# Optimization experiments

Hardware: AMD Instinct MI355X
Metric: run time of the kernel (lower is better)

Reference implementation:

```python
import jax, jax.numpy as jnp
import numpy as np

B, L, T, F, H, O = 4096, 50, 64, 3, 20, 16

def setup_inputs() -> dict:
    key = jax.random.key(0)
    ks = jax.random.split(key, 20)
    p = lambda k, s: jax.random.normal(k, s, jnp.float32) * 0.1
    inp = {
        'x': jax.random.normal(ks[0], (B, L, T, F), jnp.float32),
        'lengths': jax.random.randint(ks[1], (B, L), 0, T, jnp.int32),
        # LSTMCell params (torch gate order i,f,g,o)
        'w_ih': p(ks[2], (4 * H, F)), 'w_hh': p(ks[3], (4 * H, H)),
        'b_ih': p(ks[4], (4 * H,)), 'b_hh': p(ks[5], (4 * H,)),
        # layer-summary Linear(20,16)
        'w_lin': p(ks[6], (O, H)), 'b_lin': p(ks[7], (O,)),
        # ClassifyNet convs
        'c1_w': p(ks[8], (32, 16, 5)), 'c1_b': p(ks[9], (32,)),
        'c2_w': p(ks[10], (32, 32, 4)), 'c2_b': p(ks[11], (32,)),
        'c3_w': p(ks[12], (32, 32, 4)), 'c3_b': p(ks[13], (32,)),
        'fc1_w': p(ks[14], (16, 32 * 19)), 'fc1_b': p(ks[15], (16,)),
        'fc2_w': p(ks[16], (4, 16)), 'fc2_b': p(ks[17], (4,)),
    }
    return inp

def _conv1d(x, w, b, stride):
    y = jax.lax.conv_general_dilated(x, w, (stride,), 'VALID',
                                     dimension_numbers=('NCH', 'OIH', 'NCH'))
    return y + b[None, :, None]

def _lstm_last_h(xseq, lens, w_ih, w_hh, b_ih, b_hh):
    # xseq: [N,T,F] padded; lens: [N]. Masked batched LSTM, returns h at step len-1.
    N = xseq.shape[0]
    xT = jnp.swapaxes(xseq, 0, 1)  # [T,N,F]
    h0 = jnp.zeros((N, H), xseq.dtype)
    def step(carry, inp):
        h, c = carry
        x_t, t = inp
        gates = x_t @ w_ih.T + b_ih + h @ w_hh.T + b_hh
        i, f, g, o = jnp.split(gates, 4, axis=-1)
        c_new = jax.nn.sigmoid(f) * c + jax.nn.sigmoid(i) * jnp.tanh(g)
        h_new = jax.nn.sigmoid(o) * jnp.tanh(c_new)
        m = (t < lens)[:, None]
        return (jnp.where(m, h_new, h), jnp.where(m, c_new, c)), None
    (h, _), _ = jax.lax.scan(step, (h0, h0), (xT, jnp.arange(xT.shape[0])))
    return h

def reference(x, lengths, w_ih, w_hh, b_ih, b_hh, w_lin, b_lin,
              c1_w, c1_b, c2_w, c2_b, c3_w, c3_b, fc1_w, fc1_b, fc2_w, fc2_b):
    N = B * L
    xf = x.reshape(N, T, F)
    lens = lengths.reshape(N)
    h = _lstm_last_h(xf, lens, w_ih, w_hh, b_ih, b_hh)          # [N,20]
    summ = jax.nn.sigmoid(h @ w_lin.T + b_lin)                   # [N,16]
    summ = jnp.where((lens > 0)[:, None], summ, 0.0)             # empty layer -> zeros
    feat = jnp.swapaxes(summ.reshape(B, L, O), 1, 2)             # [B,16,50]
    y = jax.nn.relu(_conv1d(feat, c1_w, c1_b, 1))                # [B,32,46]
    y = jax.nn.relu(_conv1d(y, c2_w, c2_b, 2))                   # [B,32,22]
    y = jax.nn.relu(_conv1d(y, c3_w, c3_b, 1))                   # [B,32,19]
    y = y.reshape(B, 32 * 19)
    y = jax.nn.relu(y @ fc1_w.T + fc1_b)
    return y @ fc2_w.T + fc2_b                                   # [B,4]
```

## Files before the change

kernel.cpp:

```cpp
#include <hip/hip_runtime.h>
#include <cstdint>
#include <cstddef>

#define NB 4096
#define NL 50
#define NT 64
#define NF 3
#define NH 20
#define NO 16
#define NN (NB*NL)
#define SB 16
#define TS 16
#define HSTR 20
#define XSTR 8

typedef __attribute__((ext_vector_type(8))) short bf16x8;
typedef __attribute__((ext_vector_type(4))) float f32x4;

__device__ __forceinline__ float fsig(float z) {
    return __builtin_amdgcn_rcpf(1.0f + __expf(-z));
}
__device__ __forceinline__ unsigned short f2bf(float f) {
    unsigned int x = __float_as_uint(f);
    x = (x + 0x7fffu + ((x >> 16) & 1u)) >> 16;
    return (unsigned short)x;
}
__device__ __forceinline__ float bf2f(unsigned short u) {
    return __uint_as_float(((unsigned int)u) << 16);
}

__global__ __launch_bounds__(256) void hist_kernel(const int* __restrict__ lengths,
                                                   int* __restrict__ hist) {
    __shared__ int lh[64];
    int tid = threadIdx.x;
    if (tid < 64) lh[tid] = 0;
    __syncthreads();
    int n = blockIdx.x * 256 + tid;
    if (n < NN) {
        int len = lengths[n];
        len = len < 0 ? 0 : (len > 63 ? 63 : len);
        atomicAdd(&lh[len], 1);
    }
    __syncthreads();
    if (tid < 64 && lh[tid] != 0) atomicAdd(&hist[tid], lh[tid]);
}

__global__ void scan_kernel(const int* __restrict__ hist, int* __restrict__ cursor) {
    int l = threadIdx.x;
    int v = hist[l];
    int s = v;
#pragma unroll
    for (int d = 1; d < 64; d <<= 1) {
        int o = __shfl_up(s, d);
        if (l >= d) s += o;
    }
    cursor[l] = s - v;
}

__global__ __launch_bounds__(256) void scatter_kernel(const int* __restrict__ lengths,
                                                      int* __restrict__ cursor,
                                                      int* __restrict__ order,
                                                      int* __restrict__ len_s) {
    __shared__ int lcnt[64];
    __shared__ int lbase[64];
    int tid = threadIdx.x;
    if (tid < 64) lcnt[tid] = 0;
    __syncthreads();
    int n = blockIdx.x * 256 + tid;
    int len = 0, myrank = 0;
    if (n < NN) {
        len = lengths[n];
        len = len < 0 ? 0 : (len > 63 ? 63 : len);
        myrank = atomicAdd(&lcnt[len], 1);
    }
    __syncthreads();
    if (tid < 64 && lcnt[tid] != 0) lbase[tid] = atomicAdd(&cursor[tid], lcnt[tid]);
    __syncthreads();
    if (n < NN) {
        int pos = lbase[len] + myrank;
        order[pos] = n;
        len_s[pos] = len;
    }
}

__global__ void wfrag_kernel(const float* __restrict__ w_hh,
                             const float* __restrict__ b_ih,
                             const float* __restrict__ b_hh,
                             const float* __restrict__ w_ih,
                             unsigned int* __restrict__ wfrag) {
    int l = threadIdx.x;
    int m = l & 15, kg = l >> 4;
    for (int T = 0; T < 5; ++T) {
        int g = (m & 3) * 20 + T * 4 + (m >> 2);
        unsigned int hi[4], lo[4];
        for (int d = 0; d < 4; ++d) {
            unsigned int hw[2], lw[2];
            for (int e = 0; e < 2; ++e) {
                int k = kg * 8 + d * 2 + e;
                float v = 0.0f;
                if (k < 20)       v = w_hh[g * 20 + k];
                else if (k == 20) v = b_ih[g] + b_hh[g];
                else if (k <= 23) v = w_ih[g * 3 + (k - 21)];
                else if (k <= 26) v = w_ih[g * 3 + (k - 24)];
                unsigned short h16 = f2bf(v);
                float r = v - bf2f(h16);
                hw[e] = h16; lw[e] = f2bf(r);
            }
            hi[d] = hw[0] | (hw[1] << 16);
            lo[d] = lw[0] | (lw[1] << 16);
        }
        for (int d = 0; d < 4; ++d) {
            wfrag[(size_t)((T * 2 + 0) * 64 + l) * 4 + d] = hi[d];
            wfrag[(size_t)((T * 2 + 1) * 64 + l) * 4 + d] = lo[d];
        }
    }
}

#define LSTM_STEP(K, MASKED)                                                     \
    {                                                                            \
        uint2 ra_ = *(const uint2*)(p1 + (K) * st1);                             \
        uint2 rb_ = *(const uint2*)(p2 + (K) * st2);                             \
        union { uint4 u; bf16x8 v; } bb_;                                        \
        bb_.u = make_uint4(ra_.x, ra_.y, rb_.x, rb_.y);                          \
        f32x4 acc[5];                                                            \
        _Pragma("unroll")                                                        \
        for (int T = 0; T < 5; ++T) {                                            \
            f32x4 z4 = {0.f, 0.f, 0.f, 0.f};                                     \
            z4     = __builtin_amdgcn_mfma_f32_16x16x32_bf16(wf[2*T],   bb_.v, z4, 0, 0, 0); \
            acc[T] = __builtin_amdgcn_mfma_f32_16x16x32_bf16(wf[2*T+1], bb_.v, z4, 0, 0, 0); \
        }                                                                        \
        bool m_ = true;                                                          \
        if (MASKED) m_ = (t0 + (K)) < mylen;                                     \
        _Pragma("unroll")                                                        \
        for (int T = 0; T < 5; ++T) {                                            \
            float Ei = __expf(-acc[T][0]);                                       \
            float Ef = __expf(-acc[T][1]);                                       \
            float G  = __expf(acc[T][2] + acc[T][2]);                            \
            float Eo = __expf(-acc[T][3]);                                       \
            float Ai = 1.0f + Ei, Af = 1.0f + Ef, Bg = 1.0f + G;                 \
            float t1 = Ai * Bg;                                                  \
            float num = fmaf(G - 1.0f, Af, c5[T] * t1);                          \
            float cn  = num * __builtin_amdgcn_rcpf(t1 * Af);                    \
            float ce  = fminf(cn, 15.0f);                                        \
            float Ec  = __expf(ce + ce);                                         \
            float hn  = (Ec - 1.0f) *                                            \
                        __builtin_amdgcn_rcpf((1.0f + Eo) * (1.0f + Ec));        \
            if (m_) {                                                            \
                c5[T] = cn;                                                      \
                hbf[wid][hoff + T * 4] = f2bf(hn);                               \
            }                                                                    \
        }                                                                        \
    }

__global__ __launch_bounds__(256) void lstm_kernel(
    const float* __restrict__ x,
    const int*   __restrict__ len_s,
    const int*   __restrict__ order,
    const unsigned int* __restrict__ wfrag,
    const float* __restrict__ w_lin,
    const float* __restrict__ b_lin,
    float* __restrict__ feat)
{
    __shared__ __align__(16) unsigned short hbf[4][SB * HSTR];
    __shared__ __align__(16) unsigned short xbf[4][TS * SB * XSTR];
    __shared__ __align__(16) unsigned short zbuf[4][8];

    const int tid  = threadIdx.x;
    const int wid  = __builtin_amdgcn_readfirstlane(tid >> 6);
    const int lane = tid & 63;
    const int n16  = lane & 15;
    const int kg   = lane >> 4;
    const int base = ((gridDim.x - 1 - blockIdx.x) * 4 + wid) * SB;

    const int mylen   = len_s[base + n16];
    const int wavemin = len_s[base];
    const int wavemax = len_s[base + SB - 1];

    for (int i = lane; i < SB * HSTR; i += 64) hbf[wid][i] = 0;
    if (lane < 8) zbuf[wid][lane] = 0;
    for (int i = lane; i < TS * SB; i += 64) {
        xbf[wid][i * XSTR + 0] = 0x3F80;
        xbf[wid][i * XSTR + 7] = 0;
    }

    bf16x8 wf[10];
#pragma unroll
    for (int p = 0; p < 10; ++p) {
        union { uint4 i; bf16x8 v; } cv;
        cv.i = ((const uint4*)wfrag)[p * 64 + lane];
        wf[p] = cv.v;
    }

    int nown = order[base + n16];
    size_t gb[3]; int ssj[3], qqj[3];
#pragma unroll
    for (int j = 0; j < 3; ++j) {
        int e4 = lane + 64 * j;
        int ss = e4 / 12;
        int q  = e4 - 12 * ss;
        int ns = __shfl(nown, ss);
        gb[j] = (size_t)ns * (NT * NF) + q * 4;
        ssj[j] = ss; qqj[j] = q;
    }

    const unsigned short* hpw = &hbf[wid][n16 * HSTR];
    const unsigned short* p1 = (kg < 3) ? (hpw + kg * 8)
                                        : &xbf[wid][n16 * XSTR + 4];
    const unsigned short* p2 = (kg < 2) ? (hpw + kg * 8 + 4)
                             : (kg == 2 ? &xbf[wid][n16 * XSTR]
                                        : &zbuf[wid][0]);
    const int st1 = (kg == 3) ? SB * XSTR : 0;
    const int st2 = (kg == 2) ? SB * XSTR : 0;
    const int hoff = n16 * HSTR + kg;

    float c5[5];
#pragma unroll
    for (int j = 0; j < 5; ++j) c5[j] = 0.0f;

    if (wavemax > 0) {
        float4 vf[3];
#pragma unroll
        for (int j = 0; j < 3; ++j) vf[j] = *(const float4*)(x + gb[j]);

        for (int t0 = 0; t0 < wavemax; t0 += TS) {
#pragma unroll
            for (int j = 0; j < 3; ++j) {
                float fv4[4] = {vf[j].x, vf[j].y, vf[j].z, vf[j].w};
                int ss = ssj[j], q = qqj[j];
#pragma unroll
                for (int e = 0; e < 4; ++e) {
                    int fi = q * 4 + e;
                    int t  = fi / 3;
                    int cc = fi - 3 * t;
                    unsigned short hi = f2bf(fv4[e]);
                    unsigned short lo = f2bf(fv4[e] - bf2f(hi));
                    int bidx = (t * SB + ss) * XSTR;
                    xbf[wid][bidx + 1 + cc] = hi;
                    xbf[wid][bidx + 4 + cc] = lo;
                }
            }
            if (t0 + TS < wavemax) {
                size_t off = (size_t)(t0 + TS) * NF;
#pragma unroll
                for (int j = 0; j < 3; ++j)
                    vf[j] = *(const float4*)(x + gb[j] + off);
            }

            int kmax = wavemax - t0; if (kmax > TS) kmax = TS;
            int ku = wavemin - t0;
            ku = ku < 0 ? 0 : (ku > kmax ? kmax : ku);
            int k = 0;
            for (; k < ku; ++k)   LSTM_STEP(k, false)
            for (; k < kmax; ++k) LSTM_STEP(k, true)
        }
    }

    float hl[NH];
#pragma unroll
    for (int u = 0; u < NH; ++u) hl[u] = bf2f(hbf[wid][n16 * HSTR + u]);
    float4 res;
    if (mylen > 0) {
        float r4[4];
#pragma unroll
        for (int j = 0; j < 4; ++j) {
            int o = 4 * kg + j;
            float aa = b_lin[o];
#pragma unroll
            for (int kk = 0; kk < NH; ++kk) aa += w_lin[o * NH + kk] * hl[kk];
            r4[j] = fsig(aa);
        }
        res = make_float4(r4[0], r4[1], r4[2], r4[3]);
    } else {
        res = make_float4(0.f, 0.f, 0.f, 0.f);
    }
    *(float4*)(feat + (size_t)nown * NO + 4 * kg) = res;
}

__global__ __launch_bounds__(256) void head_kernel(
    const float* __restrict__ feat,
    const float* __restrict__ c1w, const float* __restrict__ c1b,
    const float* __restrict__ c2w, const float* __restrict__ c2b,
    const float* __restrict__ c3w, const float* __restrict__ c3b,
    const float* __restrict__ f1w, const float* __restrict__ f1b,
    const float* __restrict__ f2w, const float* __restrict__ f2b,
    float* __restrict__ out)
{
    const int b0  = blockIdx.x * 2;
    const int tid = threadIdx.x;
    const int p   = tid & 63;
    const int q   = __builtin_amdgcn_readfirstlane(tid >> 6);
    const int half = p >> 5;
    const int pp   = p & 31;

    __shared__ float sf[2][16 * 50];
    __shared__ float y1[2][32 * 46];
    __shared__ float y2[2][32 * 22];
    __shared__ float y3[2][32 * 19];
    __shared__ float r1[2][16];

    for (int i = tid; i < 2 * NL * NO; i += 256) {
        int bb = (i >= NL * NO) ? 1 : 0;
        int j = i - bb * (NL * NO);
        int l = j >> 4, o = j & 15;
        sf[bb][o * 50 + l] = feat[(size_t)(b0 + bb) * (NL * NO) + j];
    }
    __syncthreads();

    const int oc0 = q * 8;

#pragma unroll
    for (int bb = 0; bb < 2; ++bb) {
        if (p < 46) {
            float acc[8];
#pragma unroll
            for (int oc = 0; oc < 8; ++oc) acc[oc] = c1b[oc0 + oc];
#pragma unroll
            for (int ic = 0; ic < 16; ++ic) {
#pragma unroll
                for (int tap = 0; tap < 5; ++tap) {
                    float fv = sf[bb][ic * 50 + p + tap];
#pragma unroll
                    for (int oc = 0; oc < 8; ++oc)
                        acc[oc] += c1w[((oc0 + oc) * 16 + ic) * 5 + tap] * fv;
                }
            }
#pragma unroll
            for (int oc = 0; oc < 8; ++oc)
                y1[bb][(oc0 + oc) * 46 + p] = fmaxf(acc[oc], 0.0f);
        }
    }
    __syncthreads();

    if (pp < 22) {
        float acc[8];
#pragma unroll
        for (int oc = 0; oc < 8; ++oc) acc[oc] = c2b[oc0 + oc];
#pragma unroll
        for (int ic = 0; ic < 32; ++ic) {
#pragma unroll
            for (int tap = 0; tap < 4; ++tap) {
                float fv = y1[half][ic * 46 + 2 * pp + tap];
#pragma unroll
                for (int oc = 0; oc < 8; ++oc)
                    acc[oc] += c2w[((oc0 + oc) * 32 + ic) * 4 + tap] * fv;
            }
        }
#pragma unroll
        for (int oc = 0; oc < 8; ++oc)
            y2[half][(oc0 + oc) * 22 + pp] = fmaxf(acc[oc], 0.0f);
    }
    __syncthreads();

    if (pp < 19) {
        float acc[8];
#pragma unroll
        for (int oc = 0; oc < 8; ++oc) acc[oc] = c3b[oc0 + oc];
#pragma unroll
        for (int ic = 0; ic < 32; ++ic) {
#pragma unroll
            for (int tap = 0; tap < 4; ++tap) {
                float fv = y2[half][ic * 22 + pp + tap];
#pragma unroll
                for (int oc = 0; oc < 8; ++oc)
                    acc[oc] += c3w[((oc0 + oc) * 32 + ic) * 4 + tap] * fv;
            }
        }
#pragma unroll
        for (int oc = 0; oc < 8; ++oc)
            y3[half][(oc0 + oc) * 19 + pp] = fmaxf(acc[oc], 0.0f);
    }
    __syncthreads();

    if (q < 2) {
        int u  = p & 15;
        int qq = p >> 4;
        float acc = 0.0f;
        int k0 = qq * 152;
#pragma unroll 8
        for (int k = k0; k < k0 + 152; ++k) acc += f1w[u * 608 + k] * y3[q][k];
        acc += __shfl_xor(acc, 16);
        acc += __shfl_xor(acc, 32);
        if (p < 16) r1[q][p] = fmaxf(acc + f1b[p], 0.0f);
    }
    __syncthreads();

    if (q < 2 && p < 4) {
        float s = f2b[p];
#pragma unroll
        for (int k = 0; k < 16; ++k) s += f2w[p * 16 + k] * r1[q][k];
        out[(size_t)(b0 + q) * 4 + p] = s;
    }
}

extern "C" void kernel_launch(void* const* d_in, const int* in_sizes, int n_in,
                              void* d_out, int out_size, void* d_ws, size_t ws_size,
                              hipStream_t stream)
{
    const float* x     = (const float*)d_in[0];
    const int*  lengths= (const int*)  d_in[1];
    const float* w_ih  = (const float*)d_in[2];
    const float* w_hh  = (const float*)d_in[3];
    const float* b_ih  = (const float*)d_in[4];
    const float* b_hh  = (const float*)d_in[5];
    const float* w_lin = (const float*)d_in[6];
    const float* b_lin = (const float*)d_in[7];
    const float* c1w   = (const float*)d_in[8];
    const float* c1b   = (const float*)d_in[9];
    const float* c2w   = (const float*)d_in[10];
    const float* c2b   = (const float*)d_in[11];
    const float* c3w   = (const float*)d_in[12];
    const float* c3b   = (const float*)d_in[13];
    const float* f1w   = (const float*)d_in[14];
    const float* f1b   = (const float*)d_in[15];
    const float* f2w   = (const float*)d_in[16];
    const float* f2b   = (const float*)d_in[17];
    float* out = (float*)d_out;

    char* ws      = (char*)d_ws;
    float* feat   = (float*)ws;
    int*   order  = (int*)(feat + (size_t)NN * NO);
    int*   len_s  = order + NN;
    int*   hist   = len_s + NN;
    int*   cursor = hist + 64;
    unsigned int* wfrag = (unsigned int*)(cursor + 64);

    hipMemsetAsync(hist, 0, 64 * sizeof(int), stream);
    hist_kernel   <<<NN / 256, 256, 0, stream>>>(lengths, hist);
    scan_kernel   <<<1, 64, 0, stream>>>(hist, cursor);
    scatter_kernel<<<NN / 256, 256, 0, stream>>>(lengths, cursor, order, len_s);
    wfrag_kernel  <<<1, 64, 0, stream>>>(w_hh, b_ih, b_hh, w_ih, wfrag);
    lstm_kernel   <<<NN / (SB * 4), 256, 0, stream>>>(x, len_s, order, wfrag,
                                                      w_lin, b_lin, feat);
    head_kernel   <<<NB / 2, 256, 0, stream>>>(feat, c1w, c1b, c2w, c2b, c3w, c3b,
                                               f1w, f1b, f2w, f2b, out);
}
```

Measured before the change: 483.3 us.

## Fold exp2 scaling into LSTM weights, pack x staging, vectorize fc1

Pre-scales the gate weights by -log2(e), or 2·log2(e) for the g gate, so the activation code can call a bare exp2 with no negation or multiply. It also reorders the K-slot layout so x hi/lo and a constant 1 for the bias are written as one 16-byte LDS store per timestep using packed bf16 conversions, replacing many scalar stores and divides. The fc1 dot product in the classifier now uses float4 loads. Pre-scaling the weights before the bf16 hi/lo split slightly changes rounding, and the new tanh clamp bound must match the old one.

```diff
diff --git a/kernel.cpp b/kernel.cpp
--- a/kernel.cpp
+++ b/kernel.cpp
@@ -16,6 +16,18 @@
 
 typedef __attribute__((ext_vector_type(8))) short bf16x8;
 typedef __attribute__((ext_vector_type(4))) float f32x4;
+typedef uint2 u2a __attribute__((may_alias));
+typedef uint4 u4a __attribute__((may_alias));
+
+#if defined(__has_builtin)
+#  if __has_builtin(__builtin_amdgcn_exp2f)
+#    define EXP2(x) __builtin_amdgcn_exp2f(x)
+#  endif
+#endif
+#ifndef EXP2
+extern "C" __device__ float __ocml_exp2_f32(float);
+#  define EXP2(x) __ocml_exp2_f32(x)
+#endif
 
 __device__ __forceinline__ float fsig(float z) {
     return __builtin_amdgcn_rcpf(1.0f + __expf(-z));
@@ -27,6 +39,11 @@
 }
 __device__ __forceinline__ float bf2f(unsigned short u) {
     return __uint_as_float(((unsigned int)u) << 16);
+}
+__device__ __forceinline__ unsigned int cvtpk(float a, float b) {
+    unsigned int r;
+    asm("v_cvt_pk_bf16_f32 %0, %1, %2" : "=v"(r) : "v"(a), "v"(b));
+    return r;
 }
 
 __global__ __launch_bounds__(256) void hist_kernel(const int* __restrict__ lengths,
@@ -92,6 +109,8 @@
     int m = l & 15, kg = l >> 4;
     for (int T = 0; T < 5; ++T) {
         int g = (m & 3) * 20 + T * 4 + (m >> 2);
+        int jt = g / 20;
+        float sc = (jt == 2) ? 2.8853900817779268f : -1.4426950408889634f;
         unsigned int hi[4], lo[4];
         for (int d = 0; d < 4; ++d) {
             unsigned int hw[2], lw[2];
@@ -99,9 +118,10 @@
                 int k = kg * 8 + d * 2 + e;
                 float v = 0.0f;
                 if (k < 20)       v = w_hh[g * 20 + k];
-                else if (k == 20) v = b_ih[g] + b_hh[g];
-                else if (k <= 23) v = w_ih[g * 3 + (k - 21)];
+                else if (k <= 22) v = w_ih[g * 3 + (k - 20)];
+                else if (k == 23) v = b_ih[g] + b_hh[g];
                 else if (k <= 26) v = w_ih[g * 3 + (k - 24)];
+                v *= sc;
                 unsigned short h16 = f2bf(v);
                 float r = v - bf2f(h16);
                 hw[e] = h16; lw[e] = f2bf(r);
@@ -118,8 +138,8 @@
 
 #define LSTM_STEP(K, MASKED)                                                     \
     {                                                                            \
-        uint2 ra_ = *(const uint2*)(p1 + (K) * st1);                             \
-        uint2 rb_ = *(const uint2*)(p2 + (K) * st2);                             \
+        uint2 ra_ = *(const u2a*)(p1 + (K) * st1);                               \
+        uint2 rb_ = *(const u2a*)(p2 + (K) * st2);                               \
         union { uint4 u; bf16x8 v; } bb_;                                        \
         bb_.u = make_uint4(ra_.x, ra_.y, rb_.x, rb_.y);                          \
         f32x4 acc[5];                                                            \
@@ -133,16 +153,16 @@
         if (MASKED) m_ = (t0 + (K)) < mylen;                                     \
         _Pragma("unroll")                                                        \
         for (int T = 0; T < 5; ++T) {                                            \
-            float Ei = __expf(-acc[T][0]);                                       \
-            float Ef = __expf(-acc[T][1]);                                       \
-            float G  = __expf(acc[T][2] + acc[T][2]);                            \
-            float Eo = __expf(-acc[T][3]);                                       \
+            float Ei = EXP2(acc[T][0]);                            \
+            float Ef = EXP2(acc[T][1]);                            \
+            float G  = EXP2(acc[T][2]);                           \
+            float Eo = EXP2(acc[T][3]);                            \
             float Ai = 1.0f + Ei, Af = 1.0f + Ef, Bg = 1.0f + G;                 \
             float t1 = Ai * Bg;                                                  \
             float num = fmaf(G - 1.0f, Af, c5[T] * t1);                          \
             float cn  = num * __builtin_amdgcn_rcpf(t1 * Af);                    \
-            float ce  = fminf(cn, 15.0f);                                        \
-            float Ec  = __expf(ce + ce);                                         \
+            float ce2 = fminf(cn * 2.8853900817779268f, 43.3f);                  \
+            float Ec  = EXP2(ce2);                         \
             float hn  = (Ec - 1.0f) *                                            \
                         __builtin_amdgcn_rcpf((1.0f + Eo) * (1.0f + Ec));        \
             if (m_) {                                                            \
@@ -178,10 +198,6 @@
 
     for (int i = lane; i < SB * HSTR; i += 64) hbf[wid][i] = 0;
     if (lane < 8) zbuf[wid][lane] = 0;
-    for (int i = lane; i < TS * SB; i += 64) {
-        xbf[wid][i * XSTR + 0] = 0x3F80;
-        xbf[wid][i * XSTR + 7] = 0;
-    }
 
     bf16x8 wf[10];
 #pragma unroll
@@ -192,16 +208,10 @@
     }
 
     int nown = order[base + n16];
-    size_t gb[3]; int ssj[3], qqj[3];
-#pragma unroll
-    for (int j = 0; j < 3; ++j) {
-        int e4 = lane + 64 * j;
-        int ss = e4 / 12;
-        int q  = e4 - 12 * ss;
-        int ns = __shfl(nown, ss);
-        gb[j] = (size_t)ns * (NT * NF) + q * 4;
-        ssj[j] = ss; qqj[j] = q;
-    }
+    const int ssl = lane >> 2;
+    const int tq  = lane & 3;
+    int nsl = __shfl(nown, ssl);
+    const size_t gbase = (size_t)nsl * (NT * NF) + (size_t)tq * 12;
 
     const unsigned short* hpw = &hbf[wid][n16 * HSTR];
     const unsigned short* p1 = (kg < 3) ? (hpw + kg * 8)
@@ -220,30 +230,30 @@
     if (wavemax > 0) {
         float4 vf[3];
 #pragma unroll
-        for (int j = 0; j < 3; ++j) vf[j] = *(const float4*)(x + gb[j]);
+        for (int j = 0; j < 3; ++j) vf[j] = *(const float4*)(x + gbase + 4 * j);
 
         for (int t0 = 0; t0 < wavemax; t0 += TS) {
-#pragma unroll
-            for (int j = 0; j < 3; ++j) {
-                float fv4[4] = {vf[j].x, vf[j].y, vf[j].z, vf[j].w};
-                int ss = ssj[j], q = qqj[j];
-#pragma unroll
-                for (int e = 0; e < 4; ++e) {
-                    int fi = q * 4 + e;
-                    int t  = fi / 3;
-                    int cc = fi - 3 * t;
-                    unsigned short hi = f2bf(fv4[e]);
-                    unsigned short lo = f2bf(fv4[e] - bf2f(hi));
-                    int bidx = (t * SB + ss) * XSTR;
-                    xbf[wid][bidx + 1 + cc] = hi;
-                    xbf[wid][bidx + 4 + cc] = lo;
-                }
+            float f12[12] = {vf[0].x, vf[0].y, vf[0].z, vf[0].w,
+                             vf[1].x, vf[1].y, vf[1].z, vf[1].w,
+                             vf[2].x, vf[2].y, vf[2].z, vf[2].w};
+#pragma unroll
+            for (int jj = 0; jj < 4; ++jj) {
+                float a0 = f12[3 * jj], a1 = f12[3 * jj + 1], a2 = f12[3 * jj + 2];
+                unsigned int w0 = cvtpk(a0, a1);
+                unsigned int w1 = cvtpk(a2, 1.0f);
+                float r0 = a0 - __uint_as_float(w0 << 16);
+                float r1 = a1 - __uint_as_float(w0 & 0xFFFF0000u);
+                float r2 = a2 - __uint_as_float(w1 << 16);
+                unsigned int w2 = cvtpk(r0, r1);
+                unsigned int w3 = cvtpk(r2, 0.0f);
+                int t = tq * 4 + jj;
+                *(u4a*)&xbf[wid][(t * SB + ssl) * XSTR] = make_uint4(w0, w1, w2, w3);
             }
             if (t0 + TS < wavemax) {
                 size_t off = (size_t)(t0 + TS) * NF;
 #pragma unroll
                 for (int j = 0; j < 3; ++j)
-                    vf[j] = *(const float4*)(x + gb[j] + off);
+                    vf[j] = *(const float4*)(x + gbase + off + 4 * j);
             }
 
             int kmax = wavemax - t0; if (kmax > TS) kmax = TS;
@@ -295,7 +305,7 @@
     __shared__ float sf[2][16 * 50];
     __shared__ float y1[2][32 * 46];
     __shared__ float y2[2][32 * 22];
-    __shared__ float y3[2][32 * 19];
+    __shared__ __align__(16) float y3[2][32 * 19];
     __shared__ float r1[2][16];
 
     for (int i = tid; i < 2 * NL * NO; i += 256) {
@@ -374,10 +384,14 @@
     if (q < 2) {
         int u  = p & 15;
         int qq = p >> 4;
+        const float4* wv = (const float4*)(f1w + u * 608 + qq * 152);
+        const float4* yv = (const float4*)(&y3[q][qq * 152]);
         float acc = 0.0f;
-        int k0 = qq * 152;
-#pragma unroll 8
-        for (int k = k0; k < k0 + 152; ++k) acc += f1w[u * 608 + k] * y3[q][k];
+#pragma unroll 2
+        for (int k = 0; k < 38; ++k) {
+            float4 a = wv[k], bv = yv[k];
+            acc += a.x * bv.x + a.y * bv.y + a.z * bv.z + a.w * bv.w;
+        }
         acc += __shfl_xor(acc, 16);
         acc += __shfl_xor(acc, 32);
         if (p < 16) r1[q][p] = fmaxf(acc + f1b[p], 0.0f);
```

New measurement: 467.0 us. 3.4% less time.
